# Optimization experiments

Hardware: AMD Instinct MI355X
Metric: run time of the kernel (lower is better)

## Reference

```python
import jax, jax.numpy as jnp
import numpy as np

B, F, E, K, U, D_MODEL, H = 8192, 2048, 16, 2, 2048, 2048, 16
DEPTH = D_MODEL // H


def setup_inputs() -> dict:
    key = jax.random.key(0)
    ks = jax.random.split(key, 12)
    s = 0.02
    return {
        "x": jax.random.normal(ks[0], (B, F), dtype=jnp.float32),
        "router_w": jax.random.normal(ks[1], (F, E), dtype=jnp.float32) * s,
        "router_b": jnp.zeros((E,), dtype=jnp.float32),
        "expert_w": jax.random.normal(ks[2], (E, F, U), dtype=jnp.float32) * s,
        "expert_b": jnp.zeros((E, U), dtype=jnp.float32),
        "wq": jax.random.normal(ks[3], (U, D_MODEL), dtype=jnp.float32) * s,
        "bq": jnp.zeros((D_MODEL,), dtype=jnp.float32),
        "wk": jax.random.normal(ks[4], (U, D_MODEL), dtype=jnp.float32) * s,
        "bk": jnp.zeros((D_MODEL,), dtype=jnp.float32),
        "wv": jax.random.normal(ks[5], (U, D_MODEL), dtype=jnp.float32) * s,
        "bv": jnp.zeros((D_MODEL,), dtype=jnp.float32),
        "wo": jax.random.normal(ks[6], (D_MODEL, D_MODEL), dtype=jnp.float32) * s,
        "bo": jnp.zeros((D_MODEL,), dtype=jnp.float32),
    }


def reference(x, router_w, router_b, expert_w, expert_b,
              wq, bq, wk, bk, wv, bv, wo, bo):
    # ----- MoE block -----
    router_logits = x @ router_w + router_b                 # [B, E]
    router_probs = jax.nn.softmax(router_logits, axis=-1)   # [B, E]
    _, top_k_idx = jax.lax.top_k(router_probs, K)           # [B, K]
    # mask[b, e] = count of e among top-k indices of sample b (0/1 in practice)
    mask = jnp.sum(jax.nn.one_hot(top_k_idx, E, dtype=x.dtype), axis=1)  # [B, E]
    # dense all-expert compute, as in the original module
    expert_out = jax.nn.relu(jnp.einsum('bf,efu->beu', x, expert_w) + expert_b)  # [B, E, U]
    gate = router_probs * mask                               # [B, E]
    moe_out = jnp.einsum('be,beu->bu', gate, expert_out)     # [B, U]

    # ----- MLA block (elementwise attention over a single latent vector) -----
    q = (moe_out @ wq + bq).reshape(B, H, DEPTH)
    k = (moe_out @ wk + bk).reshape(B, H, DEPTH)
    v = (moe_out @ wv + bv).reshape(B, H, DEPTH)
    scores = jnp.sum(q * k, axis=-1, keepdims=True) / jnp.sqrt(jnp.float32(DEPTH))  # [B, H, 1]
    attn = jax.nn.softmax(scores, axis=-2)                   # softmax over heads
    out = (attn * v).reshape(B, H * DEPTH)                   # [B, d_model]
    return out @ wo + bo
```

## Files before the change

### kernel.cpp

```cpp
#include <hip/hip_runtime.h>
#include <hip/hip_bf16.h>
#include <cstdint>

typedef __bf16 bf16;
typedef __bf16 bf16x4 __attribute__((ext_vector_type(4)));
typedef __bf16 bf16x8 __attribute__((ext_vector_type(8)));
typedef float  f32x4  __attribute__((ext_vector_type(4)));

#define BTOK 8192
#define FDIM 2048
#define NEXP 16
#define UDIM 2048
#define DMODEL 2048
#define BSTRIDE 8320

__device__ __forceinline__ void gl2lds16(const void* g, void* l) {
  __builtin_amdgcn_global_load_lds(
      (const __attribute__((address_space(1))) void*)g,
      (__attribute__((address_space(3))) void*)l, 16, 0, 0);
}

__device__ __forceinline__ void gemm_core(
    const bf16* __restrict__ aP0, const bf16* __restrict__ aP1,
    const bf16* __restrict__ bP0, const bf16* __restrict__ bP1,
    int Kdim, bf16* As, bf16* Bs, f32x4 acc[4][4])
{
  const int tid  = threadIdx.x;
  const int lane = tid & 63;
  const int wave = tid >> 6;
  const int wm   = (wave >> 1) * 64;
  const int wn   = (wave & 1) * 64;
  const int lhi  = lane >> 4;
  const int llo  = lane & 15;
  bf16* lA0 = As + wave * 512;
  bf16* lA1 = As + 2048 + wave * 512;
  bf16* lB0 = Bs + wave * 512;
  bf16* lB1 = Bs + 2048 + wave * 512;
  for (int k0 = 0; k0 < Kdim; k0 += 32) {
    if (k0) __syncthreads();
    gl2lds16(aP0 + k0, lA0);
    gl2lds16(aP1 + k0, lA1);
    gl2lds16(bP0 + k0, lB0);
    gl2lds16(bP1 + k0, lB1);
    __syncthreads();
    bf16x8 af[4], bv[4];
#pragma unroll
    for (int i = 0; i < 4; ++i)
      af[i] = *(const bf16x8*)(As + (wm + i * 16 + llo) * 32 + lhi * 8);
#pragma unroll
    for (int j = 0; j < 4; ++j)
      bv[j] = *(const bf16x8*)(Bs + (wn + j * 16 + llo) * 32 + lhi * 8);
#pragma unroll
    for (int i = 0; i < 4; ++i)
#pragma unroll
      for (int j = 0; j < 4; ++j)
        acc[i][j] = __builtin_amdgcn_mfma_f32_16x16x32_bf16(af[i], bv[j], acc[i][j], 0, 0, 0);
  }
}


#define G256_BAR()  __builtin_amdgcn_s_barrier()
#define G256_LGK0() asm volatile("s_waitcnt lgkmcnt(0)" ::: "memory")

#define G256_STAGE(h, kt) do {                                               \
    const bf16* sb_ = ((h) < 2) ? Ab : Bb;                                   \
    const int ro_ = (((kt) & 1) << 16) + (((h) >= 2) ? 32768 : 0)            \
                    + (((h) & 1) << 13);                                     \
    _Pragma("unroll")                                                        \
    for (int l_ = 0; l_ < 2; ++l_) {                                         \
      const int u_   = (((h) & 1) << 9) + (l_ << 10) + tid;                  \
      const int row_ = (u_ & 1023) >> 2;                                     \
      const int ch_  = ((u_ >> 10) << 2)                                     \
                       + ((u_ & 3) ^ (((row_ >> 3) & 1) << 1));              \
      const bf16* s_ = sb_ + (size_t)(row_ * Kdim + (kt) * 64 + ch_ * 8);    \
      char* d_ = smem + ro_ + (l_ << 14) + ((tid & ~63) << 4);               \
      gl2lds16(s_, d_);                                                      \
    }                                                                        \
  } while (0)

#define G256_LDA(I0)                                                         \
  _Pragma("unroll") for (int i_ = 0; i_ < 4; ++i_)                           \
  _Pragma("unroll") for (int ks_ = 0; ks_ < 2; ++ks_)                        \
    Ar[(I0) + i_][ks_] =                                                     \
        *(const bf16x8*)(smem + c + aOff[(I0) + i_] + ks_ * 16384);

#define G256_LDB(J0)                                                         \
  _Pragma("unroll") for (int jj_ = 0; jj_ < 2; ++jj_)                        \
  _Pragma("unroll") for (int ks_ = 0; ks_ < 2; ++ks_)                        \
    Br[jj_][ks_] =                                                           \
        *(const bf16x8*)(smem + c + bOff[(J0) + jj_] + ks_ * 16384);

#define G256_MFMA16(I0, J0)                                                  \
  _Pragma("unroll") for (int i_ = 0; i_ < 4; ++i_)                           \
  _Pragma("unroll") for (int jj_ = 0; jj_ < 2; ++jj_)                        \
  _Pragma("unroll") for (int ks_ = 0; ks_ < 2; ++ks_)                        \
    acc[(I0) + i_][(J0) + jj_] = __builtin_amdgcn_mfma_f32_16x16x32_bf16(    \
        Ar[(I0) + i_][ks_], Br[jj_][ks_], acc[(I0) + i_][(J0) + jj_], 0, 0, 0);

template <typename OutT>
__global__ __launch_bounds__(512, 2) void gemm256(
    const bf16* __restrict__ A, const bf16* __restrict__ Bt,
    const float* __restrict__ bias, OutT* __restrict__ C,
    int M, int N, int Kdim)
{
  extern __shared__ __align__(16) char smem[];
  const int tid  = threadIdx.x;
  const int lane = tid & 63;
  const int wave = tid >> 6;
  const int wm   = (wave >> 2) << 7;
  const int wn   = (wave & 3) << 6;
  const int lhi  = lane >> 4, llo = lane & 15;

  const int nbx = N >> 8;
  const int nwg = (M >> 8) * nbx;
  const int q8  = nwg >> 3;
  const int bid = (int)blockIdx.x;
  const int swz = (bid & 7) * q8 + (bid >> 3);
  const int mBase = (swz / nbx) << 8;
  const int nBase = (swz % nbx) << 8;

  const bf16* Ab = A + (size_t)mBase * Kdim;
  const bf16* Bb = Bt + (size_t)nBase * Kdim;
  const int NT = Kdim >> 6;

  int aOff[8], bOff[4];
#pragma unroll
  for (int i = 0; i < 8; ++i) {
    const int row = wm + i * 16 + llo;
    aOff[i] = (row * 64 + lhi * 16) ^ (((row >> 3) & 1) << 5);
  }
#pragma unroll
  for (int j = 0; j < 4; ++j) {
    const int row = wn + j * 16 + llo;
    bOff[j] = 32768 + ((row * 64 + lhi * 16) ^ (((row >> 3) & 1) << 5));
  }

  f32x4 acc[8][4];
  const f32x4 zero = {0.f, 0.f, 0.f, 0.f};
#pragma unroll
  for (int i = 0; i < 8; ++i)
#pragma unroll
    for (int j = 0; j < 4; ++j) acc[i][j] = zero;

  bf16x8 Ar[8][2], Br[2][2];

  G256_STAGE(0, 0); G256_STAGE(1, 0); G256_STAGE(2, 0); G256_STAGE(3, 0);
  G256_STAGE(0, 1); G256_STAGE(1, 1);
  asm volatile("s_waitcnt vmcnt(4)" ::: "memory");
  G256_BAR();

#pragma unroll 1
  for (int t = 0; t < NT; ++t) {
    const int c = (t & 1) << 16;
    const bool p1 = (t + 1 < NT), p2 = (t + 2 < NT);
    G256_LDA(0); G256_LDB(0);
    if (p1) G256_STAGE(2, t + 1);
    G256_BAR(); G256_LGK0();
    __builtin_amdgcn_s_setprio(1); G256_MFMA16(0, 0); __builtin_amdgcn_s_setprio(0);
    G256_BAR();
    G256_LDA(4);
    if (p1) G256_STAGE(3, t + 1);
    G256_BAR(); G256_LGK0();
    __builtin_amdgcn_s_setprio(1); G256_MFMA16(4, 0); __builtin_amdgcn_s_setprio(0);
    G256_BAR();
    G256_LDB(2);
    if (p2) G256_STAGE(0, t + 2);
    G256_BAR(); G256_LGK0();
    __builtin_amdgcn_s_setprio(1); G256_MFMA16(4, 2); __builtin_amdgcn_s_setprio(0);
    G256_BAR();
    if (p2) G256_STAGE(1, t + 2);
    G256_BAR();
    __builtin_amdgcn_s_setprio(1); G256_MFMA16(0, 2); __builtin_amdgcn_s_setprio(0);
    if (p2) { asm volatile("s_waitcnt vmcnt(4)" ::: "memory"); }
    else    { asm volatile("s_waitcnt vmcnt(0)" ::: "memory"); }
    G256_BAR();
  }

#pragma unroll
  for (int i = 0; i < 8; ++i) {
#pragma unroll
    for (int r = 0; r < 4; ++r) {
      const int row = mBase + wm + i * 16 + lhi * 4 + r;
#pragma unroll
      for (int j = 0; j < 4; ++j) {
        const int col = nBase + wn + j * 16 + llo;
        C[(size_t)row * N + col] = (OutT)(acc[i][j][r] + bias[col]);
      }
    }
  }
}

__global__ __launch_bounds__(256) void transpose_kernel(
    const float* __restrict__ in, bf16* __restrict__ out,
    int R, int C, long long inZ, long long outZ)
{
  __shared__ float tile[64][65];
  const long long zi = (long long)blockIdx.z * inZ;
  const long long zo = (long long)blockIdx.z * outZ;
  const int r0 = blockIdx.y * 64, c0 = blockIdx.x * 64;
  const int tid = threadIdx.x;
  const int tr = tid >> 4;
  const int tc = (tid & 15) * 4;
#pragma unroll
  for (int it = 0; it < 4; ++it) {
    int r = it * 16 + tr;
    float4 v = *(const float4*)(in + zi + (size_t)(r0 + r) * C + c0 + tc);
    tile[r][tc] = v.x; tile[r][tc + 1] = v.y; tile[r][tc + 2] = v.z; tile[r][tc + 3] = v.w;
  }
  __syncthreads();
#pragma unroll
  for (int it = 0; it < 4; ++it) {
    int c = it * 16 + tr;
    bf16x4 ov;
    ov[0] = (bf16)tile[tc + 0][c];
    ov[1] = (bf16)tile[tc + 1][c];
    ov[2] = (bf16)tile[tc + 2][c];
    ov[3] = (bf16)tile[tc + 3][c];
    *(bf16x4*)(out + zo + (size_t)(c0 + c) * R + r0 + tc) = ov;
  }
}

__global__ __launch_bounds__(256) void concat_bias(
    const float* __restrict__ bq, const float* __restrict__ bk,
    const float* __restrict__ bv, float* __restrict__ out)
{
  int i = blockIdx.x * 256 + threadIdx.x;
  if (i < 2048) out[i] = bq[i];
  else if (i < 4096) out[i] = bk[i - 2048];
  else if (i < 6144) out[i] = bv[i - 4096];
}

__global__ __launch_bounds__(256) void router_kernel(
    const float* __restrict__ x, const float* __restrict__ rw,
    const float* __restrict__ rb, bf16* __restrict__ xb,
    int* __restrict__ cnt, int* __restrict__ btok, float* __restrict__ bgate)
{
  const int tid = threadIdx.x, lane = tid & 63, wave = tid >> 6;
  const int tokBase = blockIdx.x * 16 + wave * 4;
  float acc[4][16];
#pragma unroll
  for (int t = 0; t < 4; ++t)
#pragma unroll
    for (int e = 0; e < 16; ++e) acc[t][e] = 0.f;

#pragma unroll 1
  for (int c = 0; c < 8; ++c) {
    const int f = c * 256 + lane * 4;
    float xv[4][4];
#pragma unroll
    for (int t = 0; t < 4; ++t) {
      float4 v = *(const float4*)(x + (size_t)(tokBase + t) * FDIM + f);
      xv[t][0] = v.x; xv[t][1] = v.y; xv[t][2] = v.z; xv[t][3] = v.w;
      bf16x4 b; b[0] = (bf16)v.x; b[1] = (bf16)v.y; b[2] = (bf16)v.z; b[3] = (bf16)v.w;
      *(bf16x4*)(xb + (size_t)(tokBase + t) * FDIM + f) = b;
    }
#pragma unroll
    for (int ff = 0; ff < 4; ++ff) {
      const float* rwr = rw + (size_t)(f + ff) * 16;
      float4 r0 = *(const float4*)(rwr);
      float4 r1 = *(const float4*)(rwr + 4);
      float4 r2 = *(const float4*)(rwr + 8);
      float4 r3 = *(const float4*)(rwr + 12);
      float rr[16] = {r0.x, r0.y, r0.z, r0.w, r1.x, r1.y, r1.z, r1.w,
                      r2.x, r2.y, r2.z, r2.w, r3.x, r3.y, r3.z, r3.w};
#pragma unroll
      for (int t = 0; t < 4; ++t) {
        float xs = xv[t][ff];
#pragma unroll
        for (int e = 0; e < 16; ++e) acc[t][e] = fmaf(xs, rr[e], acc[t][e]);
      }
    }
  }
#pragma unroll
  for (int t = 0; t < 4; ++t)
#pragma unroll
    for (int e = 0; e < 16; ++e) {
      float v = acc[t][e];
      v += __shfl_xor(v, 32); v += __shfl_xor(v, 16); v += __shfl_xor(v, 8);
      v += __shfl_xor(v, 4);  v += __shfl_xor(v, 2);  v += __shfl_xor(v, 1);
      acc[t][e] = v;
    }
  if (lane < 4) {
    const int tok = tokBase + lane;
    float lg[16];
#pragma unroll
    for (int e = 0; e < 16; ++e) lg[e] = acc[lane][e] + rb[e];
    float mx = lg[0];
#pragma unroll
    for (int e = 1; e < 16; ++e) mx = fmaxf(mx, lg[e]);
    float p[16], s = 0.f;
#pragma unroll
    for (int e = 0; e < 16; ++e) { p[e] = __expf(lg[e] - mx); s += p[e]; }
    const float inv = 1.f / s;
    int e0 = 0;
#pragma unroll
    for (int e = 1; e < 16; ++e) if (lg[e] > lg[e0]) e0 = e;
    int e1 = (e0 == 0) ? 1 : 0;
#pragma unroll
    for (int e = 0; e < 16; ++e) { if (e != e0 && lg[e] > lg[e1]) e1 = e; }
    const float g0 = p[e0] * inv, g1 = p[e1] * inv;
    int s0 = atomicAdd(cnt + e0, 1);
    btok[e0 * BSTRIDE + s0] = tok; bgate[e0 * BSTRIDE + s0] = g0;
    int s1 = atomicAdd(cnt + e1, 1);
    btok[e1 * BSTRIDE + s1] = tok; bgate[e1 * BSTRIDE + s1] = g1;
  }
}

__global__ void finalize_buckets(const int* __restrict__ cnt, int* __restrict__ btok,
                                 float* __restrict__ bgate, int2* __restrict__ tmap,
                                 int* __restrict__ ntl3)
{
  __shared__ int tilesS[16];
  const int tid = threadIdx.x;
  if (tid < 16) tilesS[tid] = (cnt[tid] + 127) >> 7;
  __syncthreads();
  for (int e = 0; e < 16; ++e) {
    int c = cnt[e], end = tilesS[e] * 128;
    for (int i = c + tid; i < end; i += 256) {
      btok[e * BSTRIDE + i] = 0;
      bgate[e * BSTRIDE + i] = 0.f;
    }
  }
  if (tid == 0) {
    int s = 0, sA = 0;
    for (int e = 0; e < 16; ++e) {
      for (int m = 0; m < tilesS[e]; ++m) { tmap[s] = make_int2(e, m * 128); ++s; }
      if (e == 7) sA = s;
    }
    ntl3[0] = 0; ntl3[1] = sA; ntl3[2] = s;
  }
}

__global__ __launch_bounds__(256) void expert_gemm(
    const bf16* __restrict__ xb, const bf16* __restrict__ ewt,
    const float* __restrict__ eb, const int* __restrict__ btok,
    const float* __restrict__ bgate, const int2* __restrict__ tmap,
    const int* __restrict__ ntl3, int passIdx, int e0glob,
    float* __restrict__ moe32)
{
  __shared__ __align__(16) bf16 As[4096];
  __shared__ __align__(16) bf16 Bs[4096];
  __shared__ int   tokS[128];
  __shared__ float gateS[128];
  const int tstart = ntl3[passIdx], tend = ntl3[passIdx + 1];
  const int t = tstart + blockIdx.y;
  if (t >= tend) return;
  const int2 mp = tmap[t];
  const int e = mp.x, rowStart = mp.y;
  const int nBase = blockIdx.x * 128;
  const int tid = threadIdx.x;
  const int bbase = e * BSTRIDE + rowStart;
  if (tid < 128) {
    tokS[tid]  = btok[bbase + tid];
    gateS[tid] = bgate[bbase + tid];
  }
  const int rr0 = tid >> 2, rr1 = 64 + rr0;
  const int ch = (tid & 3) * 8;
  const int t0 = btok[bbase + rr0];
  const int t1 = btok[bbase + rr1];
  const bf16* aP0 = xb + (size_t)t0 * FDIM + ch;
  const bf16* aP1 = xb + (size_t)t1 * FDIM + ch;
  const bf16* Bb = ewt + ((size_t)(e - e0glob) << 22);
  const bf16* bP0 = Bb + (size_t)(nBase + rr0) * FDIM + ch;
  const bf16* bP1 = Bb + (size_t)(nBase + rr1) * FDIM + ch;

  f32x4 acc[4][4];
  const f32x4 zero = {0.f, 0.f, 0.f, 0.f};
#pragma unroll
  for (int i = 0; i < 4; ++i)
#pragma unroll
    for (int j = 0; j < 4; ++j) acc[i][j] = zero;

  gemm_core(aP0, aP1, bP0, bP1, FDIM, As, Bs, acc);

  const int lane = tid & 63, wave = tid >> 6;
  const int wm = (wave >> 1) * 64, wn = (wave & 1) * 64;
  const int lhi = lane >> 4, llo = lane & 15;
#pragma unroll
  for (int i = 0; i < 4; ++i) {
#pragma unroll
    for (int r = 0; r < 4; ++r) {
      const int rl = wm + i * 16 + lhi * 4 + r;
      const int tok = tokS[rl];
      const float g = gateS[rl];
      if (g != 0.f) {
#pragma unroll
        for (int j = 0; j < 4; ++j) {
          const int col = nBase + wn + j * 16 + llo;
          float v = acc[i][j][r] + eb[e * UDIM + col];
          v = fmaxf(v, 0.f);
          atomicAdd(moe32 + (size_t)tok * UDIM + col, v * g);
        }
      }
    }
  }
}

__global__ __launch_bounds__(256) void f32_to_bf16_vec(
    const float* __restrict__ in, bf16* __restrict__ out, int n4)
{
  int i = blockIdx.x * 256 + threadIdx.x;
  if (i >= n4) return;
  float4 v = ((const float4*)in)[i];
  bf16x4 b; b[0] = (bf16)v.x; b[1] = (bf16)v.y; b[2] = (bf16)v.z; b[3] = (bf16)v.w;
  ((bf16x4*)out)[i] = b;
}

__global__ __launch_bounds__(256) void attn_kernel(
    const bf16* __restrict__ qkv, bf16* __restrict__ aout)
{
  const int lane = threadIdx.x & 63, wave = threadIdx.x >> 6;
  const int tok = blockIdx.x * 4 + wave;
  const bf16* base = qkv + (size_t)tok * (3 * DMODEL);
  const int h = lane >> 2, part = lane & 3;
  const int off = h * 128 + part * 32;
  float dot = 0.f;
#pragma unroll
  for (int c = 0; c < 4; ++c) {
    bf16x8 qv = *(const bf16x8*)(base + off + c * 8);
    bf16x8 kv = *(const bf16x8*)(base + DMODEL + off + c * 8);
#pragma unroll
    for (int u = 0; u < 8; ++u) dot += (float)qv[u] * (float)kv[u];
  }
  dot += __shfl_xor(dot, 1);
  dot += __shfl_xor(dot, 2);
  const float score = dot * 0.08838834764831845f;
  float sc[16];
#pragma unroll
  for (int e = 0; e < 16; ++e) sc[e] = __shfl(score, e * 4);
  float mx = sc[0];
#pragma unroll
  for (int e = 1; e < 16; ++e) mx = fmaxf(mx, sc[e]);
  float sum = 0.f, mex = 0.f;
#pragma unroll
  for (int e = 0; e < 16; ++e) {
    float ex = __expf(sc[e] - mx);
    sum += ex;
    mex = (e == h) ? ex : mex;
  }
  const float attn = mex / sum;
  bf16* op = aout + (size_t)tok * DMODEL + off;
#pragma unroll
  for (int c = 0; c < 4; ++c) {
    bf16x8 vv = *(const bf16x8*)(base + 2 * DMODEL + off + c * 8);
    bf16x8 ov;
#pragma unroll
    for (int u = 0; u < 8; ++u) ov[u] = (bf16)(attn * (float)vv[u]);
    *(bf16x8*)(op + c * 8) = ov;
  }
}

extern "C" void kernel_launch(void* const* d_in, const int* in_sizes, int n_in,
                              void* d_out, int out_size, void* d_ws, size_t ws_size,
                              hipStream_t stream) {
  const float* x   = (const float*)d_in[0];
  const float* rw  = (const float*)d_in[1];
  const float* rb  = (const float*)d_in[2];
  const float* ew  = (const float*)d_in[3];
  const float* eb  = (const float*)d_in[4];
  const float* wq  = (const float*)d_in[5];
  const float* bq  = (const float*)d_in[6];
  const float* wk  = (const float*)d_in[7];
  const float* bk  = (const float*)d_in[8];
  const float* wv  = (const float*)d_in[9];
  const float* bv  = (const float*)d_in[10];
  const float* wo_ = (const float*)d_in[11];
  const float* bo  = (const float*)d_in[12];
  float* out = (float*)d_out;

  static bool attrSet = false;
  if (!attrSet) {
    hipFuncSetAttribute((const void*)gemm256<bf16>,
                        hipFuncAttributeMaxDynamicSharedMemorySize, 131072);
    hipFuncSetAttribute((const void*)gemm256<float>,
                        hipFuncAttributeMaxDynamicSharedMemorySize, 131072);
    attrSet = true;
  }

  uint8_t* ws = (uint8_t*)d_ws;
  bf16*  ewt   = (bf16*)(ws);
  bf16*  moeb  = (bf16*)(ws);
  bf16*  aout  = (bf16*)(ws);
  float* moe32 = (float*)(ws + 67108864);
  bf16*  qkv   = (bf16*)(ws + 67108864);
  bf16*  xb    = (bf16*)(ws + 167772160);
  bf16*  qkvt  = (bf16*)(ws + 167772160);
  bf16*  wot   = (bf16*)(ws + 167772160 + 25165824);
  uint8_t* misc = ws + 201326592;
  float* bqkv  = (float*)(misc);            misc += 24576;
  int*   cnt   = (int*)(misc);              misc += 256;
  int*   ntl3  = (int*)(misc);              misc += 256;
  int2*  tmap  = (int2*)(misc);             misc += 2048;
  int*   btok  = (int*)(misc);              misc += 532480;
  float* bgate = (float*)(misc);            misc += 532480;

  hipMemsetAsync(moe32, 0, 67108864, stream);
  hipMemsetAsync(cnt, 0, 64, stream);

  transpose_kernel<<<dim3(32, 32, 8), 256, 0, stream>>>(ew, ewt, FDIM, UDIM, 4194304LL, 4194304LL);
  router_kernel<<<512, 256, 0, stream>>>(x, rw, rb, xb, cnt, btok, bgate);
  finalize_buckets<<<1, 256, 0, stream>>>(cnt, btok, bgate, tmap, ntl3);
  expert_gemm<<<dim3(16, 136), 256, 0, stream>>>(xb, ewt, eb, btok, bgate, tmap, ntl3, 0, 0, moe32);
  transpose_kernel<<<dim3(32, 32, 8), 256, 0, stream>>>(ew + (size_t)8 * 4194304, ewt, FDIM, UDIM, 4194304LL, 4194304LL);
  expert_gemm<<<dim3(16, 136), 256, 0, stream>>>(xb, ewt, eb, btok, bgate, tmap, ntl3, 1, 8, moe32);

  f32_to_bf16_vec<<<16384, 256, 0, stream>>>(moe32, moeb, 4194304);

  transpose_kernel<<<dim3(32, 32, 1), 256, 0, stream>>>(wq, qkvt,            UDIM, DMODEL, 0, 0);
  transpose_kernel<<<dim3(32, 32, 1), 256, 0, stream>>>(wk, qkvt + 4194304,  UDIM, DMODEL, 0, 0);
  transpose_kernel<<<dim3(32, 32, 1), 256, 0, stream>>>(wv, qkvt + 8388608,  UDIM, DMODEL, 0, 0);
  transpose_kernel<<<dim3(32, 32, 1), 256, 0, stream>>>(wo_, wot, DMODEL, DMODEL, 0, 0);
  concat_bias<<<24, 256, 0, stream>>>(bq, bk, bv, bqkv);

  gemm256<bf16><<<dim3(768), 512, 131072, stream>>>(moeb, qkvt, bqkv, qkv, BTOK, 3 * DMODEL, UDIM);
  attn_kernel<<<2048, 256, 0, stream>>>(qkv, aout);
  gemm256<float><<<dim3(256), 512, 131072, stream>>>(aout, wot, bo, out, BTOK, DMODEL, 2048);
}
```

Before: 1.293 ms.

## Use 256x256 pipelined expert GEMM with bf16 slot output and gather-combine

Replaces the small 128x128 expert GEMM, which scattered gated results into an fp32 buffer with atomics, with a 256x256 tile kernel that reuses the pipelined gemm256 k-loop and gathers token rows by index. Each expert tile writes relu(xW+b) in bf16 to per-slot rows, and a new combine kernel reads each token's two slot rows and applies the gate weights. This drops the 64MB memset, the fp32 atomics and the separate fp32-to-bf16 conversion. In exchange it adds an intermediate bf16 buffer, pads buckets to 256 rows (more wasted rows), and needs a gather-combine pass.

```diff
diff --git a/kernel.cpp b/kernel.cpp
--- a/kernel.cpp
+++ b/kernel.cpp
@@ -12,50 +12,12 @@
 #define NEXP 16
 #define UDIM 2048
 #define DMODEL 2048
-#define BSTRIDE 8320
+#define BSTRIDE 8448
 
 __device__ __forceinline__ void gl2lds16(const void* g, void* l) {
   __builtin_amdgcn_global_load_lds(
       (const __attribute__((address_space(1))) void*)g,
       (__attribute__((address_space(3))) void*)l, 16, 0, 0);
-}
-
-__device__ __forceinline__ void gemm_core(
-    const bf16* __restrict__ aP0, const bf16* __restrict__ aP1,
-    const bf16* __restrict__ bP0, const bf16* __restrict__ bP1,
-    int Kdim, bf16* As, bf16* Bs, f32x4 acc[4][4])
-{
-  const int tid  = threadIdx.x;
-  const int lane = tid & 63;
-  const int wave = tid >> 6;
-  const int wm   = (wave >> 1) * 64;
-  const int wn   = (wave & 1) * 64;
-  const int lhi  = lane >> 4;
-  const int llo  = lane & 15;
-  bf16* lA0 = As + wave * 512;
-  bf16* lA1 = As + 2048 + wave * 512;
-  bf16* lB0 = Bs + wave * 512;
-  bf16* lB1 = Bs + 2048 + wave * 512;
-  for (int k0 = 0; k0 < Kdim; k0 += 32) {
-    if (k0) __syncthreads();
-    gl2lds16(aP0 + k0, lA0);
-    gl2lds16(aP1 + k0, lA1);
-    gl2lds16(bP0 + k0, lB0);
-    gl2lds16(bP1 + k0, lB1);
-    __syncthreads();
-    bf16x8 af[4], bv[4];
-#pragma unroll
-    for (int i = 0; i < 4; ++i)
-      af[i] = *(const bf16x8*)(As + (wm + i * 16 + llo) * 32 + lhi * 8);
-#pragma unroll
-    for (int j = 0; j < 4; ++j)
-      bv[j] = *(const bf16x8*)(Bs + (wn + j * 16 + llo) * 32 + lhi * 8);
-#pragma unroll
-    for (int i = 0; i < 4; ++i)
-#pragma unroll
-      for (int j = 0; j < 4; ++j)
-        acc[i][j] = __builtin_amdgcn_mfma_f32_16x16x32_bf16(af[i], bv[j], acc[i][j], 0, 0, 0);
-  }
 }
 
 
@@ -78,6 +40,19 @@
     }                                                                        \
   } while (0)
 
+#define E256_STAGE(h, kt) do {                                               \
+    const bf16* rp_ = ((h) == 0) ? aRow0 : ((h) == 1) ? aRow1                \
+                      : ((h) == 2) ? bRow0 : bRow1;                          \
+    const int ro_ = (((kt) & 1) << 16) + (((h) >= 2) ? 32768 : 0)            \
+                    + (((h) & 1) << 13);                                     \
+    _Pragma("unroll")                                                        \
+    for (int l_ = 0; l_ < 2; ++l_) {                                         \
+      const bf16* s_ = rp_ + (kt) * 64 + (l_ * 4 + chsw) * 8;                \
+      char* d_ = smem + ro_ + (l_ << 14) + ((tid & ~63) << 4);               \
+      gl2lds16(s_, d_);                                                      \
+    }                                                                        \
+  } while (0)
+
 #define G256_LDA(I0)                                                         \
   _Pragma("unroll") for (int i_ = 0; i_ < 4; ++i_)                           \
   _Pragma("unroll") for (int ks_ = 0; ks_ < 2; ++ks_)                        \
@@ -96,6 +71,51 @@
   _Pragma("unroll") for (int ks_ = 0; ks_ < 2; ++ks_)                        \
     acc[(I0) + i_][(J0) + jj_] = __builtin_amdgcn_mfma_f32_16x16x32_bf16(    \
         Ar[(I0) + i_][ks_], Br[jj_][ks_], acc[(I0) + i_][(J0) + jj_], 0, 0, 0);
+
+#define G256_OFFSETS()                                                       \
+  int aOff[8], bOff[4];                                                      \
+  _Pragma("unroll")                                                          \
+  for (int i = 0; i < 8; ++i) {                                              \
+    const int row = wm + i * 16 + llo;                                       \
+    aOff[i] = (row * 64 + lhi * 16) ^ (((row >> 3) & 1) << 5);               \
+  }                                                                          \
+  _Pragma("unroll")                                                          \
+  for (int j = 0; j < 4; ++j) {                                              \
+    const int row = wn + j * 16 + llo;                                       \
+    bOff[j] = 32768 + ((row * 64 + lhi * 16) ^ (((row >> 3) & 1) << 5));     \
+  }
+
+#define G256_KLOOP(STAGE_M, NT)                                              \
+  STAGE_M(0, 0); STAGE_M(1, 0); STAGE_M(2, 0); STAGE_M(3, 0);                \
+  STAGE_M(0, 1); STAGE_M(1, 1);                                              \
+  asm volatile("s_waitcnt vmcnt(4)" ::: "memory");                           \
+  G256_BAR();                                                                \
+  _Pragma("unroll 1")                                                        \
+  for (int t = 0; t < (NT); ++t) {                                           \
+    const int c = (t & 1) << 16;                                             \
+    const bool p1 = (t + 1 < (NT)), p2 = (t + 2 < (NT));                     \
+    G256_LDA(0); G256_LDB(0);                                                \
+    if (p1) STAGE_M(2, t + 1);                                               \
+    G256_BAR(); G256_LGK0();                                                 \
+    __builtin_amdgcn_s_setprio(1); G256_MFMA16(0, 0); __builtin_amdgcn_s_setprio(0); \
+    G256_BAR();                                                              \
+    G256_LDA(4);                                                             \
+    if (p1) STAGE_M(3, t + 1);                                               \
+    G256_BAR(); G256_LGK0();                                                 \
+    __builtin_amdgcn_s_setprio(1); G256_MFMA16(4, 0); __builtin_amdgcn_s_setprio(0); \
+    G256_BAR();                                                              \
+    G256_LDB(2);                                                             \
+    if (p2) STAGE_M(0, t + 2);                                               \
+    G256_BAR(); G256_LGK0();                                                 \
+    __builtin_amdgcn_s_setprio(1); G256_MFMA16(4, 2); __builtin_amdgcn_s_setprio(0); \
+    G256_BAR();                                                              \
+    if (p2) STAGE_M(1, t + 2);                                               \
+    G256_BAR();                                                              \
+    __builtin_amdgcn_s_setprio(1); G256_MFMA16(0, 2); __builtin_amdgcn_s_setprio(0); \
+    if (p2) { asm volatile("s_waitcnt vmcnt(4)" ::: "memory"); }             \
+    else    { asm volatile("s_waitcnt vmcnt(0)" ::: "memory"); }             \
+    G256_BAR();                                                              \
+  }
 
 template <typename OutT>
 __global__ __launch_bounds__(512, 2) void gemm256(
@@ -123,17 +143,7 @@
   const bf16* Bb = Bt + (size_t)nBase * Kdim;
   const int NT = Kdim >> 6;
 
-  int aOff[8], bOff[4];
-#pragma unroll
-  for (int i = 0; i < 8; ++i) {
-    const int row = wm + i * 16 + llo;
-    aOff[i] = (row * 64 + lhi * 16) ^ (((row >> 3) & 1) << 5);
-  }
-#pragma unroll
-  for (int j = 0; j < 4; ++j) {
-    const int row = wn + j * 16 + llo;
-    bOff[j] = 32768 + ((row * 64 + lhi * 16) ^ (((row >> 3) & 1) << 5));
-  }
+  G256_OFFSETS();
 
   f32x4 acc[8][4];
   const f32x4 zero = {0.f, 0.f, 0.f, 0.f};
@@ -144,37 +154,7 @@
 
   bf16x8 Ar[8][2], Br[2][2];
 
-  G256_STAGE(0, 0); G256_STAGE(1, 0); G256_STAGE(2, 0); G256_STAGE(3, 0);
-  G256_STAGE(0, 1); G256_STAGE(1, 1);
-  asm volatile("s_waitcnt vmcnt(4)" ::: "memory");
-  G256_BAR();
-
-#pragma unroll 1
-  for (int t = 0; t < NT; ++t) {
-    const int c = (t & 1) << 16;
-    const bool p1 = (t + 1 < NT), p2 = (t + 2 < NT);
-    G256_LDA(0); G256_LDB(0);
-    if (p1) G256_STAGE(2, t + 1);
-    G256_BAR(); G256_LGK0();
-    __builtin_amdgcn_s_setprio(1); G256_MFMA16(0, 0); __builtin_amdgcn_s_setprio(0);
-    G256_BAR();
-    G256_LDA(4);
-    if (p1) G256_STAGE(3, t + 1);
-    G256_BAR(); G256_LGK0();
-    __builtin_amdgcn_s_setprio(1); G256_MFMA16(4, 0); __builtin_amdgcn_s_setprio(0);
-    G256_BAR();
-    G256_LDB(2);
-    if (p2) G256_STAGE(0, t + 2);
-    G256_BAR(); G256_LGK0();
-    __builtin_amdgcn_s_setprio(1); G256_MFMA16(4, 2); __builtin_amdgcn_s_setprio(0);
-    G256_BAR();
-    if (p2) G256_STAGE(1, t + 2);
-    G256_BAR();
-    __builtin_amdgcn_s_setprio(1); G256_MFMA16(0, 2); __builtin_amdgcn_s_setprio(0);
-    if (p2) { asm volatile("s_waitcnt vmcnt(4)" ::: "memory"); }
-    else    { asm volatile("s_waitcnt vmcnt(0)" ::: "memory"); }
-    G256_BAR();
-  }
+  G256_KLOOP(G256_STAGE, NT);
 
 #pragma unroll
   for (int i = 0; i < 8; ++i) {
@@ -188,6 +168,85 @@
       }
     }
   }
+}
+
+__global__ __launch_bounds__(512, 2) void expert_gemm256(
+    const bf16* __restrict__ xb, const bf16* __restrict__ ewt,
+    const float* __restrict__ eb, const int* __restrict__ btok,
+    const int2* __restrict__ tmap, const int* __restrict__ ntl3,
+    const int* __restrict__ slotBase, int passIdx, int e0glob,
+    bf16* __restrict__ eout)
+{
+  extern __shared__ __align__(16) char smem[];
+  const int tstart = ntl3[passIdx], tend = ntl3[passIdx + 1];
+  const int t = tstart + (int)blockIdx.y;
+  if (t >= tend) return;
+  const int2 mp = tmap[t];
+  const int e = mp.x, rowStart = mp.y;
+  const int nBase = (int)blockIdx.x << 8;
+  const int tid  = threadIdx.x;
+  const int lane = tid & 63;
+  const int wave = tid >> 6;
+  const int wm   = (wave >> 2) << 7;
+  const int wn   = (wave & 3) << 6;
+  const int lhi  = lane >> 4, llo = lane & 15;
+
+  const int r0 = tid >> 2;
+  const int bbase = e * BSTRIDE + rowStart;
+  const bf16* aRow0 = xb + (size_t)btok[bbase + r0] * FDIM;
+  const bf16* aRow1 = xb + (size_t)btok[bbase + 128 + r0] * FDIM;
+  const bf16* Bb = ewt + ((size_t)(e - e0glob) << 22);
+  const bf16* bRow0 = Bb + (size_t)(nBase + r0) * FDIM;
+  const bf16* bRow1 = Bb + (size_t)(nBase + 128 + r0) * FDIM;
+  const int chsw = (tid & 3) ^ (((r0 >> 3) & 1) << 1);
+
+  G256_OFFSETS();
+
+  f32x4 acc[8][4];
+  const f32x4 zero = {0.f, 0.f, 0.f, 0.f};
+#pragma unroll
+  for (int i = 0; i < 8; ++i)
+#pragma unroll
+    for (int j = 0; j < 4; ++j) acc[i][j] = zero;
+
+  bf16x8 Ar[8][2], Br[2][2];
+
+  G256_KLOOP(E256_STAGE, 32);
+
+  const int orow = slotBase[e] + rowStart;
+#pragma unroll
+  for (int i = 0; i < 8; ++i) {
+#pragma unroll
+    for (int r = 0; r < 4; ++r) {
+      const int row = orow + wm + i * 16 + lhi * 4 + r;
+#pragma unroll
+      for (int j = 0; j < 4; ++j) {
+        const int col = nBase + wn + j * 16 + llo;
+        const float v = fmaxf(acc[i][j][r] + eb[e * UDIM + col], 0.f);
+        eout[(size_t)row * UDIM + col] = (bf16)v;
+      }
+    }
+  }
+}
+
+__global__ __launch_bounds__(256) void moe_combine(
+    const bf16* __restrict__ eout, const int* __restrict__ pidx,
+    const float* __restrict__ tgate, const int* __restrict__ slotBase,
+    bf16* __restrict__ moeb)
+{
+  const int tok = blockIdx.x;
+  const int p0 = pidx[2 * tok], p1 = pidx[2 * tok + 1];
+  const int r0 = slotBase[p0 >> 14] + (p0 & 16383);
+  const int r1 = slotBase[p1 >> 14] + (p1 & 16383);
+  const float g0 = tgate[2 * tok], g1 = tgate[2 * tok + 1];
+  const int cb = threadIdx.x * 8;
+  bf16x8 a = *(const bf16x8*)(eout + (size_t)r0 * UDIM + cb);
+  bf16x8 b = *(const bf16x8*)(eout + (size_t)r1 * UDIM + cb);
+  bf16x8 o;
+#pragma unroll
+  for (int u = 0; u < 8; ++u)
+    o[u] = (bf16)(g0 * (float)a[u] + g1 * (float)b[u]);
+  *(bf16x8*)(moeb + (size_t)tok * UDIM + cb) = o;
 }
 
 __global__ __launch_bounds__(256) void transpose_kernel(
@@ -233,7 +292,8 @@
 __global__ __launch_bounds__(256) void router_kernel(
     const float* __restrict__ x, const float* __restrict__ rw,
     const float* __restrict__ rb, bf16* __restrict__ xb,
-    int* __restrict__ cnt, int* __restrict__ btok, float* __restrict__ bgate)
+    int* __restrict__ cnt, int* __restrict__ btok,
+    int* __restrict__ pidx, float* __restrict__ tgate)
 {
   const int tid = threadIdx.x, lane = tid & 63, wave = tid >> 6;
   const int tokBase = blockIdx.x * 16 + wave * 4;
@@ -300,110 +360,38 @@
     for (int e = 0; e < 16; ++e) { if (e != e0 && lg[e] > lg[e1]) e1 = e; }
     const float g0 = p[e0] * inv, g1 = p[e1] * inv;
     int s0 = atomicAdd(cnt + e0, 1);
-    btok[e0 * BSTRIDE + s0] = tok; bgate[e0 * BSTRIDE + s0] = g0;
+    btok[e0 * BSTRIDE + s0] = tok;
+    pidx[2 * tok]     = (e0 << 14) | s0;
+    tgate[2 * tok]    = g0;
     int s1 = atomicAdd(cnt + e1, 1);
-    btok[e1 * BSTRIDE + s1] = tok; bgate[e1 * BSTRIDE + s1] = g1;
+    btok[e1 * BSTRIDE + s1] = tok;
+    pidx[2 * tok + 1] = (e1 << 14) | s1;
+    tgate[2 * tok + 1] = g1;
   }
 }
 
 __global__ void finalize_buckets(const int* __restrict__ cnt, int* __restrict__ btok,
-                                 float* __restrict__ bgate, int2* __restrict__ tmap,
-                                 int* __restrict__ ntl3)
+                                 int2* __restrict__ tmap, int* __restrict__ ntl3,
+                                 int* __restrict__ slotBase)
 {
   __shared__ int tilesS[16];
   const int tid = threadIdx.x;
-  if (tid < 16) tilesS[tid] = (cnt[tid] + 127) >> 7;
+  if (tid < 16) tilesS[tid] = (cnt[tid] + 255) >> 8;
   __syncthreads();
   for (int e = 0; e < 16; ++e) {
-    int c = cnt[e], end = tilesS[e] * 128;
-    for (int i = c + tid; i < end; i += 256) {
-      btok[e * BSTRIDE + i] = 0;
-      bgate[e * BSTRIDE + i] = 0.f;
-    }
+    int c = cnt[e], end = tilesS[e] << 8;
+    for (int i = c + tid; i < end; i += 256) btok[e * BSTRIDE + i] = 0;
   }
   if (tid == 0) {
-    int s = 0, sA = 0;
+    int s = 0, sA = 0, sb = 0;
     for (int e = 0; e < 16; ++e) {
-      for (int m = 0; m < tilesS[e]; ++m) { tmap[s] = make_int2(e, m * 128); ++s; }
+      slotBase[e] = sb;
+      for (int m = 0; m < tilesS[e]; ++m) { tmap[s] = make_int2(e, m << 8); ++s; }
+      sb += tilesS[e] << 8;
       if (e == 7) sA = s;
     }
     ntl3[0] = 0; ntl3[1] = sA; ntl3[2] = s;
   }
-}
-
-__global__ __launch_bounds__(256) void expert_gemm(
-    const bf16* __restrict__ xb, const bf16* __restrict__ ewt,
-    const float* __restrict__ eb, const int* __restrict__ btok,
-    const float* __restrict__ bgate, const int2* __restrict__ tmap,
-    const int* __restrict__ ntl3, int passIdx, int e0glob,
-    float* __restrict__ moe32)
-{
-  __shared__ __align__(16) bf16 As[4096];
-  __shared__ __align__(16) bf16 Bs[4096];
-  __shared__ int   tokS[128];
-  __shared__ float gateS[128];
-  const int tstart = ntl3[passIdx], tend = ntl3[passIdx + 1];
-  const int t = tstart + blockIdx.y;
-  if (t >= tend) return;
-  const int2 mp = tmap[t];
-  const int e = mp.x, rowStart = mp.y;
-  const int nBase = blockIdx.x * 128;
-  const int tid = threadIdx.x;
-  const int bbase = e * BSTRIDE + rowStart;
-  if (tid < 128) {
-    tokS[tid]  = btok[bbase + tid];
-    gateS[tid] = bgate[bbase + tid];
-  }
-  const int rr0 = tid >> 2, rr1 = 64 + rr0;
-  const int ch = (tid & 3) * 8;
-  const int t0 = btok[bbase + rr0];
-  const int t1 = btok[bbase + rr1];
-  const bf16* aP0 = xb + (size_t)t0 * FDIM + ch;
-  const bf16* aP1 = xb + (size_t)t1 * FDIM + ch;
-  const bf16* Bb = ewt + ((size_t)(e - e0glob) << 22);
-  const bf16* bP0 = Bb + (size_t)(nBase + rr0) * FDIM + ch;
-  const bf16* bP1 = Bb + (size_t)(nBase + rr1) * FDIM + ch;
-
-  f32x4 acc[4][4];
-  const f32x4 zero = {0.f, 0.f, 0.f, 0.f};
-#pragma unroll
-  for (int i = 0; i < 4; ++i)
-#pragma unroll
-    for (int j = 0; j < 4; ++j) acc[i][j] = zero;
-
-  gemm_core(aP0, aP1, bP0, bP1, FDIM, As, Bs, acc);
-
-  const int lane = tid & 63, wave = tid >> 6;
-  const int wm = (wave >> 1) * 64, wn = (wave & 1) * 64;
-  const int lhi = lane >> 4, llo = lane & 15;
-#pragma unroll
-  for (int i = 0; i < 4; ++i) {
-#pragma unroll
-    for (int r = 0; r < 4; ++r) {
-      const int rl = wm + i * 16 + lhi * 4 + r;
-      const int tok = tokS[rl];
-      const float g = gateS[rl];
-      if (g != 0.f) {
-#pragma unroll
-        for (int j = 0; j < 4; ++j) {
-          const int col = nBase + wn + j * 16 + llo;
-          float v = acc[i][j][r] + eb[e * UDIM + col];
-          v = fmaxf(v, 0.f);
-          atomicAdd(moe32 + (size_t)tok * UDIM + col, v * g);
-        }
-      }
-    }
-  }
-}
-
-__global__ __launch_bounds__(256) void f32_to_bf16_vec(
-    const float* __restrict__ in, bf16* __restrict__ out, int n4)
-{
-  int i = blockIdx.x * 256 + threadIdx.x;
-  if (i >= n4) return;
-  float4 v = ((const float4*)in)[i];
-  bf16x4 b; b[0] = (bf16)v.x; b[1] = (bf16)v.y; b[2] = (bf16)v.z; b[3] = (bf16)v.w;
-  ((bf16x4*)out)[i] = b;
 }
 
 __global__ __launch_bounds__(256) void attn_kernel(
@@ -474,6 +462,8 @@
                         hipFuncAttributeMaxDynamicSharedMemorySize, 131072);
     hipFuncSetAttribute((const void*)gemm256<float>,
                         hipFuncAttributeMaxDynamicSharedMemorySize, 131072);
+    hipFuncSetAttribute((const void*)expert_gemm256,
+                        hipFuncAttributeMaxDynamicSharedMemorySize, 131072);
     attrSet = true;
   }
 
@@ -481,7 +471,7 @@
   bf16*  ewt   = (bf16*)(ws);
   bf16*  moeb  = (bf16*)(ws);
   bf16*  aout  = (bf16*)(ws);
-  float* moe32 = (float*)(ws + 67108864);
+  bf16*  eout  = (bf16*)(ws + 67108864);
   bf16*  qkv   = (bf16*)(ws + 67108864);
   bf16*  xb    = (bf16*)(ws + 167772160);
   bf16*  qkvt  = (bf16*)(ws + 167772160);
@@ -490,21 +480,22 @@
   float* bqkv  = (float*)(misc);            misc += 24576;
   int*   cnt   = (int*)(misc);              misc += 256;
   int*   ntl3  = (int*)(misc);              misc += 256;
+  int*   slotBase = (int*)(misc);           misc += 256;
   int2*  tmap  = (int2*)(misc);             misc += 2048;
-  int*   btok  = (int*)(misc);              misc += 532480;
-  float* bgate = (float*)(misc);            misc += 532480;
-
-  hipMemsetAsync(moe32, 0, 67108864, stream);
+  int*   btok  = (int*)(misc);              misc += 540672;
+  int*   pidx  = (int*)(misc);              misc += 65536;
+  float* tgate = (float*)(misc);            misc += 65536;
+
   hipMemsetAsync(cnt, 0, 64, stream);
 
   transpose_kernel<<<dim3(32, 32, 8), 256, 0, stream>>>(ew, ewt, FDIM, UDIM, 4194304LL, 4194304LL);
-  router_kernel<<<512, 256, 0, stream>>>(x, rw, rb, xb, cnt, btok, bgate);
-  finalize_buckets<<<1, 256, 0, stream>>>(cnt, btok, bgate, tmap, ntl3);
-  expert_gemm<<<dim3(16, 136), 256, 0, stream>>>(xb, ewt, eb, btok, bgate, tmap, ntl3, 0, 0, moe32);
+  router_kernel<<<512, 256, 0, stream>>>(x, rw, rb, xb, cnt, btok, pidx, tgate);
+  finalize_buckets<<<1, 256, 0, stream>>>(cnt, btok, tmap, ntl3, slotBase);
+  expert_gemm256<<<dim3(8, 72), 512, 131072, stream>>>(xb, ewt, eb, btok, tmap, ntl3, slotBase, 0, 0, eout);
   transpose_kernel<<<dim3(32, 32, 8), 256, 0, stream>>>(ew + (size_t)8 * 4194304, ewt, FDIM, UDIM, 4194304LL, 4194304LL);
-  expert_gemm<<<dim3(16, 136), 256, 0, stream>>>(xb, ewt, eb, btok, bgate, tmap, ntl3, 1, 8, moe32);
-
-  f32_to_bf16_vec<<<16384, 256, 0, stream>>>(moe32, moeb, 4194304);
+  expert_gemm256<<<dim3(8, 72), 512, 131072, stream>>>(xb, ewt, eb, btok, tmap, ntl3, slotBase, 1, 8, eout);
+
+  moe_combine<<<8192, 256, 0, stream>>>(eout, pidx, tgate, slotBase, moeb);
 
   transpose_kernel<<<dim3(32, 32, 1), 256, 0, stream>>>(wq, qkvt,            UDIM, DMODEL, 0, 0);
   transpose_kernel<<<dim3(32, 32, 1), 256, 0, stream>>>(wk, qkvt + 4194304,  UDIM, DMODEL, 0, 0);
```

New measurement: 1.121 ms. 1.15x faster.
